# Kernel tuning notes

Measured on AMD Instinct MI355X. Metric: run time of the kernel, lower is better.

Reference implementation:

```python
import jax, jax.numpy as jnp
import numpy as np

K = 17  # pk + 1 (self + 16 neighbors)
NEG_SLOPE = 0.01  # torch LeakyReLU default


def knn_idx(points, k):
    # points: [B, 3, N]; returns nearest-neighbor indices [B, N, k], self first
    inner = -2.0 * jnp.einsum('bcn,bcm->bnm', points, points)
    xx = jnp.sum(points * points, axis=1)  # [B, N]
    pairwise = -xx[:, :, None] - inner - xx[:, None, :]  # -||pi - pj||^2
    _, idx = jax.lax.top_k(pairwise, k)  # largest = nearest; [B, N, k]
    return idx


def gather_edge_features(x, idx):
    # x: [B, C, N], idx: [B, N, k] -> [B, C, k, N]
    g = jax.vmap(lambda xb, ib: xb[:, ib])(x, idx)  # [B, C, N, k]
    return jnp.transpose(g, (0, 1, 3, 2))


def setup_inputs() -> dict:
    key = jax.random.key(0)
    ks = jax.random.split(key, 16)
    B, N = 2, 8192
    Cl, Cg = 64, 1024
    Cef_in = Cl + 3          # 67
    Cmlp_in = Cg + Cl + 128 + 3  # 1219

    def w(k, shape, fan_in):
        return jax.random.normal(k, shape, dtype=jnp.float32) * (1.0 / np.sqrt(fan_in))

    return {
        'global_feat': jax.random.normal(ks[0], (B, Cg), dtype=jnp.float32),
        'points': jax.random.normal(ks[1], (B, 3, N), dtype=jnp.float32),
        'local_feats': jax.random.normal(ks[2], (B, Cl, N), dtype=jnp.float32),
        'W_ef1': w(ks[3], (256, Cef_in), Cef_in),
        'b_ef1': jnp.zeros((256,), jnp.float32),
        'W_ef2': w(ks[4], (128, 256), 256),
        'b_ef2': jnp.zeros((128,), jnp.float32),
        'W1': w(ks[5], (1024, Cmlp_in), Cmlp_in),
        'b1': jnp.zeros((1024,), jnp.float32),
        'W2': w(ks[6], (256, 1024), 1024),
        'b2': jnp.zeros((256,), jnp.float32),
        'W3': w(ks[7], (1, 256), 256),
        'b3': jnp.zeros((1,), jnp.float32),
    }


def reference(global_feat, points, local_feats, W_ef1, b_ef1, W_ef2, b_ef2,
              W1, b1, W2, b2, W3, b3):
    B, _, N = points.shape
    idx = knn_idx(points, K)                       # [B, N, K]
    x_knn = gather_edge_features(points, idx)      # [B, 3, K, N]
    f_knn = gather_edge_features(local_feats, idx) # [B, Cl, K, N]
    # minus_xyz_center=True: center-relative coords for neighbors (skip self slot 0)
    x_knn = jnp.concatenate(
        [x_knn[:, :, :1, :], points[:, :, None, :] - x_knn[:, :, 1:, :]], axis=2)
    # with_xyz=True
    f = jnp.concatenate([f_knn, x_knn], axis=1)    # [B, Cl+3, K, N]
    # ef_mlp: 1x1 Conv2d -> LeakyReLU -> 1x1 Conv2d
    h = jnp.einsum('oc,bckn->bokn', W_ef1, f) + b_ef1[None, :, None, None]
    h = jax.nn.leaky_relu(h, NEG_SLOPE)
    h = jnp.einsum('oc,bckn->bokn', W_ef2, h) + b_ef2[None, :, None, None]
    f_max = jnp.max(h, axis=2)                     # [B, 128, N]
    g = jnp.broadcast_to(global_feat[:, :, None], (B, global_feat.shape[1], N))
    feature = jnp.concatenate([g, local_feats, f_max, points], axis=1)  # [B, 1219, N]
    # mlp: 1x1 Conv1d stack
    y = jnp.einsum('oc,bcn->bon', W1, feature) + b1[None, :, None]
    y = jax.nn.leaky_relu(y, NEG_SLOPE)
    y = jnp.einsum('oc,bcn->bon', W2, y) + b2[None, :, None]
    y = jax.nn.leaky_relu(y, NEG_SLOPE)
    out = jnp.einsum('oc,bcn->bon', W3, y) + b3[None, :, None]  # [B, 1, N]
    return out
```

## Files before the change

### kernel.cpp

```cpp
#include <hip/hip_runtime.h>
#include <hip/hip_bf16.h>
#include <cstdint>

#define B 2
#define N 8192
#define KTOT 17
#define CL 64
#define CEF 67
#define H1 256
#define H2 128
#define CG 1024
#define O1 1024
#define O2 256
#define NCHW 8
#define WCH 256
#define KPAIR 9

typedef unsigned long long u64;
typedef __bf16 bf16x8 __attribute__((ext_vector_type(8)));
typedef float f32x4 __attribute__((ext_vector_type(4)));

__device__ __forceinline__ float lrelu(float v) { return fmaxf(v, 0.01f * v); }

__device__ __forceinline__ unsigned short f2bf(float f) {
    union { float f; unsigned u; } v; v.f = f;
    unsigned r = v.u + 0x7FFFu + ((v.u >> 16) & 1u);
    return (unsigned short)(r >> 16);
}

__device__ __forceinline__ unsigned cvt_pk_bf16(float lo, float hi) {
    unsigned r;
    asm("v_cvt_pk_bf16_f32 %0, %1, %2" : "=v"(r) : "v"(lo), "v"(hi));
    return r;
}

__device__ __forceinline__ float norm3(float x, float y, float z) {
    return __fmaf_rn(z, z, __fmaf_rn(y, y, __fmul_rn(x, x)));
}
__device__ __forceinline__ float dist_key(float qx, float qy, float qz, float qq,
                                          float4 c) {
    float dot = __fmaf_rn(qz, c.z, __fmaf_rn(qy, c.y, __fmul_rn(qx, c.x)));
    float t = __fmaf_rn(-2.f, dot, qq);
    return fmaxf(__fadd_rn(t, c.w), 0.f);
}

__device__ __forceinline__ int nbucket(float nn) {
    return (int)fminf(nn * 16.f, 255.f);
}

__global__ void prep_cand4_hist(const float* __restrict__ pts, float4* __restrict__ cand4,
                                unsigned* __restrict__ hist) {
    int id = blockIdx.x * 256 + threadIdx.x;
    int b = id >> 13, j = id & (N - 1);
    const float* px = pts + (size_t)b * 3 * N;
    float x = px[j], y = px[N + j], z = px[2 * N + j];
    float nn = norm3(x, y, z);
    cand4[id] = make_float4(x, y, z, nn);
    atomicAdd(&hist[b * 256 + nbucket(nn)], 1u);
}

__global__ void knn_prefix(const unsigned* __restrict__ hist, unsigned* __restrict__ boff) {
    __shared__ unsigned s[256];
    int t = threadIdx.x;
    for (int b = 0; b < B; ++b) {
        s[t] = hist[b * 256 + t];
        __syncthreads();
        for (int d = 1; d < 256; d <<= 1) {
            unsigned v = (t >= d) ? s[t - d] : 0u;
            __syncthreads();
            s[t] += v;
            __syncthreads();
        }
        boff[b * 256 + t] = s[t] - hist[b * 256 + t];
        __syncthreads();
    }
}
__global__ void knn_scatter(const float4* __restrict__ cand4, unsigned* __restrict__ boff,
                            float4* __restrict__ cand4s, int* __restrict__ sortidx) {
    int id = blockIdx.x * 256 + threadIdx.x;
    int b = id >> 13, j = id & (N - 1);
    float4 c = cand4[id];
    unsigned pos = atomicAdd(&boff[b * 256 + nbucket(c.w)], 1u);
    cand4s[(size_t)b * N + pos] = c;
    sortidx[b * N + pos] = j;
}

#define S1 24576
#define S2 32768
#define S3 229376
#define S4 262144
__global__ void prepack_all(const float* __restrict__ W_ef1, const float* __restrict__ W_ef2,
                            const float* __restrict__ W1, const float* __restrict__ W2,
                            unsigned short* __restrict__ W1p, unsigned short* __restrict__ W2p,
                            unsigned short* __restrict__ W1m, unsigned short* __restrict__ W2m) {
    int id = blockIdx.x * 256 + threadIdx.x;
    if (id < S1) {
        int j = id & 7, l = (id >> 3) & 63, rest = id >> 9;
        int ks = rest % 3, mt = rest / 3;
        int m = mt * 16 + (l & 15);
        int k = ks * 32 + ((l >> 4) << 3) + j;
        W1p[id] = f2bf((k < CEF) ? W_ef1[m * CEF + k] : 0.f);
        return;
    }
    id -= S1;
    if (id < S2) {
        int j = id & 7, l = (id >> 3) & 63, rest = id >> 9;
        int ks = rest & 7, mt = rest >> 3;
        int m = mt * 16 + (l & 15);
        int k = ks * 32 + ((l >> 4) << 3) + j;
        W2p[id] = f2bf(W_ef2[m * H1 + k]);
        return;
    }
    id -= S2;
    if (id < S3) {
        int j = id & 7, l = (id >> 3) & 63, rest = id >> 9;
        int ks = rest % 7; int rest2 = rest / 7;
        int mt = rest2 & 3, w = (rest2 >> 2) & 3, ch = rest2 >> 4;
        int m = ch * 256 + w * 64 + mt * 16 + (l & 15);
        int k = ks * 32 + ((l >> 4) << 3) + j;
        W1m[id] = (k < 195) ? f2bf(W1[(size_t)m * 1219 + 1024 + k]) : (unsigned short)0;
        return;
    }
    id -= S3;
    if (id < S4) {
        int j = id & 7, l = (id >> 3) & 63, rest = id >> 9;
        int ks = rest & 7; int rest2 = rest >> 3;
        int mt = rest2 & 3, w = (rest2 >> 2) & 3, ch = rest2 >> 4;
        int m = w * 64 + mt * 16 + (l & 15);
        int k = ch * 256 + ks * 32 + ((l >> 4) << 3) + j;
        W2m[id] = f2bf(W2[(size_t)m * 1024 + k]);
    }
}

__global__ void prep_lf_bf(const float* __restrict__ lf, unsigned short* __restrict__ out) {
    int id = blockIdx.x * 256 + threadIdx.x;
    int c = id & 63;
    int n = (id >> 6) & (N - 1);
    int b = id >> 19;
    out[id] = f2bf(lf[((size_t)b * CL + c) * N + n]);
}

__global__ __launch_bounds__(256) void gvec_kernel(const float* __restrict__ W1,
                                                   const float* __restrict__ b1,
                                                   const float* __restrict__ g,
                                                   float* __restrict__ gvec) {
    const int t = threadIdx.x;
    const int l = t & 63;
    const int o = blockIdx.x * 4 + (t >> 6);
    const int b = blockIdx.y;
    const float* row = W1 + (size_t)o * 1219;
    const float* gb = g + b * CG;
    float s = 0.f;
#pragma unroll
    for (int i = 0; i < CG / 64; ++i)
        s = fmaf(row[l + i * 64], gb[l + i * 64], s);
    s += __shfl_xor(s, 1);  s += __shfl_xor(s, 2);  s += __shfl_xor(s, 4);
    s += __shfl_xor(s, 8);  s += __shfl_xor(s, 16); s += __shfl_xor(s, 32);
    if (l == 0) gvec[b * O1 + o] = s + b1[o];
}

__global__ __launch_bounds__(256) void knn_pass1w(const float4* __restrict__ cand4s,
                                                  float* __restrict__ topd) {
    const int t = threadIdx.x;
    const int x = blockIdx.x;
    const int chunk = blockIdx.y;
    const int b = blockIdx.z;
    int wstart = x * 256 - 896;
    wstart = wstart < 0 ? 0 : (wstart > N - 2048 ? N - 2048 : wstart);
    const int p = x * 256 + t;
    const int rel = p - wstart - chunk * WCH;
    const float4 q = cand4s[(size_t)b * N + p];
    const float qq = q.w;
    const float4* cb = cand4s + (size_t)b * N + wstart + chunk * WCH;
    float qd[16];
#pragma unroll
    for (int r = 0; r < 16; ++r) qd[r] = __builtin_inff();
#pragma unroll 8
    for (int s = 0; s < WCH; ++s) {
        float key = dist_key(q.x, q.y, q.z, qq, cb[s]);
        if (s == rel) key = __builtin_inff();
#pragma unroll
        for (int r = 15; r >= 1; --r)
            qd[r] = __builtin_amdgcn_fmed3f(key, qd[r - 1], qd[r]);
        qd[0] = fminf(key, qd[0]);
    }
#pragma unroll
    for (int s = 0; s < 16; ++s)
        topd[(size_t)((b * NCHW + chunk) * 16 + s) * N + p] = qd[s];
}

__global__ __launch_bounds__(256) void knn_thresh(const float* __restrict__ topd,
                                                  float* __restrict__ Tbuf) {
    const int t = threadIdx.x;
    const int i = blockIdx.x * 256 + t;
    const int b = blockIdx.y;
    float qd[16];
#pragma unroll
    for (int s = 0; s < 16; ++s)
        qd[s] = topd[(size_t)((b * NCHW + 0) * 16 + s) * N + i];
    for (int c = 1; c < NCHW; ++c) {
        for (int s = 0; s < 16; ++s) {
            float pk = topd[(size_t)((b * NCHW + c) * 16 + s) * N + i];
            if (pk >= qd[15]) break;
#pragma unroll
            for (int r = 15; r >= 1; --r)
                qd[r] = __builtin_amdgcn_fmed3f(pk, qd[r - 1], qd[r]);
            qd[0] = fminf(pk, qd[0]);
        }
    }
    Tbuf[b * N + i] = qd[15];
}

__global__ __launch_bounds__(256) void knn_recover(const float4* __restrict__ cand4s,
                                                   const int* __restrict__ sortidx,
                                                   const float* __restrict__ Tbuf,
                                                   const unsigned* __restrict__ boff,
                                                   int* __restrict__ idx) {
    const int t = threadIdx.x;
    const int lg = t & 15;
    const int grp = t >> 4;
    const int b = blockIdx.y;
    const int pq = blockIdx.x * 16 + grp;
    __shared__ u64 cbuf[16][64];
    __shared__ unsigned obuf[16][17];
    __shared__ int scnt[16];
    if (lg == 0) scnt[grp] = 0;
    __syncthreads();
    const int gq = sortidx[b * N + pq];
    const float4 q = cand4s[(size_t)b * N + pq];
    const float qq = q.w;
    const float T = Tbuf[b * N + pq];
    const float nq = sqrtf(qq);
    const float r = sqrtf(T) * 1.001f + 0.01f;
    const float lov = (nq > r) ? (nq - r) * (nq - r) : 0.f;
    const float hiv = (nq + r) * (nq + r);
    const int lob = nbucket(lov), hib = nbucket(hiv);
    const int start = (lob == 0) ? 0 : (int)boff[b * 256 + lob - 1];
    const int end = (int)boff[b * 256 + hib];
    const float4* cs = cand4s + (size_t)b * N;
    const int* si = sortidx + b * N;
    const int last = end - 1;
    for (int pos = start + lg; pos < end; pos += 64) {
        int p1 = pos + 16, p2 = pos + 32, p3 = pos + 48;
        float4 c0 = cs[pos];
        float4 c1 = cs[p1 < end ? p1 : last];
        float4 c2 = cs[p2 < end ? p2 : last];
        float4 c3 = cs[p3 < end ? p3 : last];
        float k0 = dist_key(q.x, q.y, q.z, qq, c0);
        float k1 = dist_key(q.x, q.y, q.z, qq, c1);
        float k2 = dist_key(q.x, q.y, q.z, qq, c2);
        float k3 = dist_key(q.x, q.y, q.z, qq, c3);
        if (k0 <= T) {
            int j = si[pos];
            if (j != gq) { int p = atomicAdd(&scnt[grp], 1); if (p < 64) cbuf[grp][p] = ((u64)__float_as_uint(k0) << 32) | (unsigned)j; }
        }
        if (k1 <= T && p1 < end) {
            int j = si[p1];
            if (j != gq) { int p = atomicAdd(&scnt[grp], 1); if (p < 64) cbuf[grp][p] = ((u64)__float_as_uint(k1) << 32) | (unsigned)j; }
        }
        if (k2 <= T && p2 < end) {
            int j = si[p2];
            if (j != gq) { int p = atomicAdd(&scnt[grp], 1); if (p < 64) cbuf[grp][p] = ((u64)__float_as_uint(k2) << 32) | (unsigned)j; }
        }
        if (k3 <= T && p3 < end) {
            int j = si[p3];
            if (j != gq) { int p = atomicAdd(&scnt[grp], 1); if (p < 64) cbuf[grp][p] = ((u64)__float_as_uint(k3) << 32) | (unsigned)j; }
        }
    }
    __syncthreads();
    int cnt = scnt[grp]; if (cnt > 64) cnt = 64;
    u64 mine[4]; bool have[4]; int rank[4];
#pragma unroll
    for (int e = 0; e < 4; ++e) {
        int pi = lg + e * 16;
        have[e] = pi < cnt;
        mine[e] = have[e] ? cbuf[grp][pi] : ~0ull;
        rank[e] = 0;
    }
    for (int m = 0; m < cnt; ++m) {
        u64 v = cbuf[grp][m];
#pragma unroll
        for (int e = 0; e < 4; ++e) rank[e] += (v < mine[e]) ? 1 : 0;
    }
    obuf[grp][1 + lg] = (unsigned)gq;
    __syncthreads();
#pragma unroll
    for (int e = 0; e < 4; ++e)
        if (have[e] && rank[e] < 16)
            obuf[grp][1 + rank[e]] = (unsigned)(mine[e] & 0xFFFFFFFFu);
    if (lg == 0) obuf[grp][0] = (unsigned)gq;
    __syncthreads();
    int* op = idx + (size_t)(b * N + gq) * KTOT;
    op[lg] = (int)obuf[grp][lg];
    if (lg == 0) op[16] = (int)obuf[grp][16];
}

__global__ __launch_bounds__(256) void ef_mlp_mfma(
        const unsigned short* __restrict__ lfb16, const float4* __restrict__ cand4,
        const int* __restrict__ idx,
        const unsigned short* __restrict__ W1p, const float* __restrict__ b_ef1,
        const unsigned short* __restrict__ W2p, const float* __restrict__ b_ef2,
        unsigned short* __restrict__ fmax_bf) {
    const int t = threadIdx.x;
    const int w = t >> 6;
    const int l = t & 63;
    const int n0 = blockIdx.x * 16;
    const int b = blockIdx.y;

    __shared__ unsigned short f_lds[32][104];
    __shared__ unsigned short h1_lds[32][264];
    __shared__ int idx_l[16][17];

    for (int e = t; e < 16 * 17; e += 256) {
        int p = e / 17, k = e - p * 17;
        idx_l[p][k] = idx[(size_t)(b * N + n0 + p) * KTOT + k];
    }
    for (int e = t; e < 32 * 29; e += 256) {
        int col = e / 29, rr = 67 + e % 29;
        f_lds[col][rr] = 0;
    }

    f32x4 b1i[4];
#pragma unroll
    for (int mt = 0; mt < 4; ++mt)
#pragma unroll
        for (int r = 0; r < 4; ++r)
            b1i[mt][r] = b_ef1[(w * 4 + mt) * 16 + ((l >> 4) << 2) + r];
    f32x4 b2i[2];
#pragma unroll
    for (int i = 0; i < 2; ++i)
#pragma unroll
        for (int r = 0; r < 4; ++r)
            b2i[i][r] = b_ef2[(w * 2 + i) * 16 + ((l >> 4) << 2) + r];

    bf16x8 A1[12];
#pragma unroll
    for (int mt = 0; mt < 4; ++mt)
#pragma unroll
        for (int ks = 0; ks < 3; ++ks)
            A1[mt * 3 + ks] = *(const bf16x8*)(W1p + (size_t)(((w * 4 + mt) * 3 + ks) * 64 + l) * 8);
    bf16x8 A2[16];
#pragma unroll
    for (int i = 0; i < 2; ++i)
#pragma unroll
        for (int ks = 0; ks < 8; ++ks)
            A2[i * 8 + ks] = *(const bf16x8*)(W2p + (size_t)(((w * 2 + i) * 8 + ks) * 64 + l) * 8);

    const int p_my = t >> 4;
    const int cbr = (t & 15) * 4;
    const unsigned short* lfb = lfb16 + (size_t)b * N * 64;
    const float4* cand4b = cand4 + (size_t)b * N;
    float selfp = 0.f;
    if (t < 48) selfp = ((const float*)(cand4b + n0 + (t & 15)))[t >> 4];

    __syncthreads();

    uint2 rbf[2];
    float rp[2];
    auto prefetch = [&](int g) {
#pragma unroll
        for (int sl = 0; sl < 2; ++sl) {
            int kk = 2 * g + sl; if (kk > 16) kk = 16;
            int j = idx_l[p_my][kk];
            rbf[sl] = *(const uint2*)(lfb + (size_t)j * 64 + cbr);
        }
        if (t < 48) {
#pragma unroll
            for (int sl = 0; sl < 2; ++sl) {
                int kk = 2 * g + sl; if (kk > 16) kk = 16;
                int j = idx_l[t & 15][kk];
                rp[sl] = ((const float*)(cand4b + j))[t >> 4];
            }
        }
    };
    auto commit = [&](int g) {
#pragma unroll
        for (int sl = 0; sl < 2; ++sl)
            *(uint2*)&f_lds[sl * 16 + p_my][cbr] = rbf[sl];
        if (t < 48) {
#pragma unroll
            for (int sl = 0; sl < 2; ++sl) {
                int kk = 2 * g + sl; if (kk > 16) kk = 16;
                float v = (kk == 0) ? selfp : selfp - rp[sl];
                f_lds[sl * 16 + (t & 15)][64 + (t >> 4)] = f2bf(v);
            }
        }
    };

    prefetch(0);
    f32x4 rmax[2];
#pragma unroll
    for (int i = 0; i < 2; ++i)
#pragma unroll
        for (int r = 0; r < 4; ++r) rmax[i][r] = -1e30f;

    for (int g = 0; g < KPAIR; ++g) {
        commit(g);
        __syncthreads();
        if (g < KPAIR - 1) prefetch(g + 1);
        f32x4 acc1[4][2];
#pragma unroll
        for (int mt = 0; mt < 4; ++mt)
#pragma unroll
            for (int nt = 0; nt < 2; ++nt) acc1[mt][nt] = b1i[mt];
#pragma unroll
        for (int nt = 0; nt < 2; ++nt) {
            const int col = nt * 16 + (l & 15);
            bf16x8 Bf0 = *(const bf16x8*)&f_lds[col][(l >> 4) * 8];
            bf16x8 Bf1 = *(const bf16x8*)&f_lds[col][32 + (l >> 4) * 8];
            bf16x8 Bf2 = *(const bf16x8*)&f_lds[col][64 + (l >> 4) * 8];
#pragma unroll
            for (int mt = 0; mt < 4; ++mt) {
                acc1[mt][nt] = __builtin_amdgcn_mfma_f32_16x16x32_bf16(A1[mt * 3 + 0], Bf0, acc1[mt][nt], 0, 0, 0);
                acc1[mt][nt] = __builtin_amdgcn_mfma_f32_16x16x32_bf16(A1[mt * 3 + 1], Bf1, acc1[mt][nt], 0, 0, 0);
                acc1[mt][nt] = __builtin_amdgcn_mfma_f32_16x16x32_bf16(A1[mt * 3 + 2], Bf2, acc1[mt][nt], 0, 0, 0);
            }
        }
#pragma unroll
        for (int mt = 0; mt < 4; ++mt)
#pragma unroll
            for (int nt = 0; nt < 2; ++nt) {
                uint2 d;
                d.x = cvt_pk_bf16(lrelu(acc1[mt][nt][0]), lrelu(acc1[mt][nt][1]));
                d.y = cvt_pk_bf16(lrelu(acc1[mt][nt][2]), lrelu(acc1[mt][nt][3]));
                *(uint2*)&h1_lds[nt * 16 + (l & 15)][(w * 4 + mt) * 16 + ((l >> 4) << 2)] = d;
            }
        __syncthreads();
        f32x4 acc2[2][2];
#pragma unroll
        for (int i = 0; i < 2; ++i)
#pragma unroll
            for (int nt = 0; nt < 2; ++nt) acc2[i][nt] = b2i[i];
#pragma unroll
        for (int nt = 0; nt < 2; ++nt) {
            const int col = nt * 16 + (l & 15);
#pragma unroll
            for (int ks = 0; ks < 8; ++ks) {
                bf16x8 Bf = *(const bf16x8*)&h1_lds[col][ks * 32 + (l >> 4) * 8];
                acc2[0][nt] = __builtin_amdgcn_mfma_f32_16x16x32_bf16(A2[0 * 8 + ks], Bf, acc2[0][nt], 0, 0, 0);
                acc2[1][nt] = __builtin_amdgcn_mfma_f32_16x16x32_bf16(A2[1 * 8 + ks], Bf, acc2[1][nt], 0, 0, 0);
            }
        }
#pragma unroll
        for (int i = 0; i < 2; ++i)
#pragma unroll
            for (int nt = 0; nt < 2; ++nt)
#pragma unroll
                for (int r = 0; r < 4; ++r)
                    rmax[i][r] = fmaxf(rmax[i][r], acc2[i][nt][r]);
    }
    const size_t nbase = ((size_t)(b * N + n0 + (l & 15))) * H2;
#pragma unroll
    for (int i = 0; i < 2; ++i) {
        uint2 d;
        d.x = cvt_pk_bf16(rmax[i][0], rmax[i][1]);
        d.y = cvt_pk_bf16(rmax[i][2], rmax[i][3]);
        *(uint2*)&fmax_bf[nbase + (w * 2 + i) * 16 + ((l >> 4) << 2)] = d;
    }
}

__global__ __launch_bounds__(512) void mlp_mfma(
        const unsigned short* __restrict__ lfb16, const float* __restrict__ pts,
        const unsigned short* __restrict__ fmax_bf, const float* __restrict__ gvec,
        const unsigned short* __restrict__ W1m, const unsigned short* __restrict__ W2m,
        const float* __restrict__ W3, const float* __restrict__ b2v,
        const float* __restrict__ b3v, float* __restrict__ out) {
    const int t = threadIdx.x;
    const int w2 = t >> 6;
    const int l = t & 63;
    const int ow = w2 >> 1;
    const int n0 = blockIdx.x * 32;
    const int b = blockIdx.y;

    __shared__ unsigned short feat_s[32 * 256];
    __shared__ unsigned short y1c_s[32 * 256];
    __shared__ float red[8][32];

    auto sw = [](int n, int cbyte) -> unsigned {
        return (unsigned)(n << 9) | ((unsigned)cbyte ^ (((unsigned)n & 7u) << 4));
    };
    char* featB = (char*)feat_s;
    char* y1cB = (char*)y1c_s;

    const unsigned short* lfb = lfb16 + (size_t)b * N * 64;
    for (int e = t; e < 32 * 64; e += 512) {
        int c = e & 63, n = e >> 6;
        *(unsigned short*)(featB + sw(n, c * 2)) = lfb[(size_t)(n0 + n) * 64 + c];
    }
    for (int e = t; e < 32 * 128; e += 512) {
        int c = e & 127, n = e >> 7;
        *(unsigned short*)(featB + sw(n, (64 + c) * 2)) =
            fmax_bf[((size_t)(b * N + n0 + n)) * H2 + c];
    }
    if (t < 96) {
        int n = t & 31, d = t >> 5;
        *(unsigned short*)(featB + sw(n, (192 + d) * 2)) =
            f2bf(pts[((size_t)(b * 3 + d)) * N + n0 + n]);
    }
    for (int e = t; e < 32 * 29; e += 512) {
        int n = e / 29, c = 195 + e % 29;
        *(unsigned short*)(featB + sw(n, c * 2)) = 0;
    }
    __syncthreads();

    f32x4 accB[2][2];
#pragma unroll
    for (int mt = 0; mt < 2; ++mt)
#pragma unroll
        for (int nt = 0; nt < 2; ++nt)
            accB[mt][nt] = (f32x4){0.f, 0.f, 0.f, 0.f};

    for (int ch = 0; ch < 4; ++ch) {
        bf16x8 A1[2][7];
#pragma unroll
        for (int mt = 0; mt < 2; ++mt) {
            const int omt = (w2 & 1) * 2 + mt;
#pragma unroll
            for (int ks = 0; ks < 7; ++ks)
                A1[mt][ks] = *(const bf16x8*)(W1m +
                    (size_t)((((ch * 4 + ow) * 4 + omt) * 7 + ks) * 64 + l) * 8);
        }
        f32x4 accA[2][2];
#pragma unroll
        for (int mt = 0; mt < 2; ++mt) {
            const int m = w2 * 32 + mt * 16 + ((l >> 4) << 2);
            const f32x4 gv = *(const f32x4*)(gvec + b * O1 + ch * 256 + m);
#pragma unroll
            for (int nt = 0; nt < 2; ++nt)
                accA[mt][nt] = gv;
        }
#pragma unroll
        for (int nt = 0; nt < 2; ++nt) {
            const int n = nt * 16 + (l & 15);
#pragma unroll
            for (int ks = 0; ks < 7; ++ks) {
                bf16x8 Bf = *(const bf16x8*)(featB + sw(n, ks * 64 + (l >> 4) * 16));
#pragma unroll
                for (int mt = 0; mt < 2; ++mt)
                    accA[mt][nt] = __builtin_amdgcn_mfma_f32_16x16x32_bf16(
                        A1[mt][ks], Bf, accA[mt][nt], 0, 0, 0);
            }
        }
        bf16x8 A2[2][8];
#pragma unroll
        for (int mt = 0; mt < 2; ++mt) {
            const int omt = (w2 & 1) * 2 + mt;
#pragma unroll
            for (int ks = 0; ks < 8; ++ks)
                A2[mt][ks] = *(const bf16x8*)(W2m +
                    (size_t)((((ch * 4 + ow) * 4 + omt) * 8 + ks) * 64 + l) * 8);
        }
        if (ch) __syncthreads();
#pragma unroll
        for (int mt = 0; mt < 2; ++mt) {
            const int m = w2 * 32 + mt * 16 + ((l >> 4) << 2);
#pragma unroll
            for (int nt = 0; nt < 2; ++nt) {
                const int n = nt * 16 + (l & 15);
                uint2 d;
                d.x = cvt_pk_bf16(lrelu(accA[mt][nt][0]), lrelu(accA[mt][nt][1]));
                d.y = cvt_pk_bf16(lrelu(accA[mt][nt][2]), lrelu(accA[mt][nt][3]));
                *(uint2*)(y1cB + sw(n, m * 2)) = d;
            }
        }
        __syncthreads();
#pragma unroll
        for (int nt = 0; nt < 2; ++nt) {
            const int n = nt * 16 + (l & 15);
#pragma unroll
            for (int ks = 0; ks < 8; ++ks) {
                bf16x8 Bf = *(const bf16x8*)(y1cB + sw(n, ks * 64 + (l >> 4) * 16));
#pragma unroll
                for (int mt = 0; mt < 2; ++mt)
                    accB[mt][nt] = __builtin_amdgcn_mfma_f32_16x16x32_bf16(
                        A2[mt][ks], Bf, accB[mt][nt], 0, 0, 0);
            }
        }
    }

    float p0 = 0.f, p1 = 0.f;
#pragma unroll
    for (int mt = 0; mt < 2; ++mt) {
        const int m = w2 * 32 + mt * 16 + ((l >> 4) << 2);
        const f32x4 bb = *(const f32x4*)(b2v + m);
        const f32x4 w3 = *(const f32x4*)(W3 + m);
#pragma unroll
        for (int r = 0; r < 4; ++r) {
            p0 = fmaf(w3[r], lrelu(accB[mt][0][r] + bb[r]), p0);
            p1 = fmaf(w3[r], lrelu(accB[mt][1][r] + bb[r]), p1);
        }
    }
    p0 += __shfl_xor(p0, 16); p0 += __shfl_xor(p0, 32);
    p1 += __shfl_xor(p1, 16); p1 += __shfl_xor(p1, 32);
    if (l < 16) { red[w2][l] = p0; red[w2][16 + l] = p1; }
    __syncthreads();
    if (t < 32) {
        float s = b3v[0];
#pragma unroll
        for (int ww = 0; ww < 8; ++ww) s += red[ww][t];
        out[(size_t)b * N + n0 + t] = s;
    }
}

extern "C" void kernel_launch(void* const* d_in, const int* in_sizes, int n_in,
                              void* d_out, int out_size, void* d_ws, size_t ws_size,
                              hipStream_t stream) {
    const float* g     = (const float*)d_in[0];
    const float* pts   = (const float*)d_in[1];
    const float* lf    = (const float*)d_in[2];
    const float* W_ef1 = (const float*)d_in[3];
    const float* b_ef1 = (const float*)d_in[4];
    const float* W_ef2 = (const float*)d_in[5];
    const float* b_ef2 = (const float*)d_in[6];
    const float* W1    = (const float*)d_in[7];
    const float* b1    = (const float*)d_in[8];
    const float* W2    = (const float*)d_in[9];
    const float* b2    = (const float*)d_in[10];
    const float* W3    = (const float*)d_in[11];
    const float* b3    = (const float*)d_in[12];
    float* out = (float*)d_out;

    char* ws = (char*)d_ws;
    int*      idx     = (int*)ws;     ws += (size_t)B * N * KTOT * 4;
    float4*   cand4   = (float4*)ws;  ws += (size_t)B * N * 16;
    float4*   cand4s  = (float4*)ws;  ws += (size_t)B * N * 16;
    int*      sortidx = (int*)ws;     ws += (size_t)B * N * 4;
    unsigned* hist    = (unsigned*)ws; ws += (size_t)B * 256 * 4;
    unsigned* boff    = (unsigned*)ws; ws += (size_t)B * 256 * 4;
    float*    topd    = (float*)ws;
    unsigned short* fmax_bf = (unsigned short*)topd;
    ws += (size_t)B * NCHW * 16 * N * 4;
    float*    Tbuf  = (float*)ws;    ws += (size_t)B * N * 4;
    float*    gvec  = (float*)ws;    ws += (size_t)B * O1 * 4;
    unsigned short* lfb16 = (unsigned short*)ws; ws += (size_t)B * N * 64 * 2;
    unsigned short* W1p = (unsigned short*)ws; ws += (size_t)S1 * 2;
    unsigned short* W2p = (unsigned short*)ws; ws += (size_t)S2 * 2;
    unsigned short* W1m = (unsigned short*)ws; ws += (size_t)S3 * 2;
    unsigned short* W2m = (unsigned short*)ws; ws += (size_t)S4 * 2;

    hipMemsetAsync(hist, 0, (size_t)B * 256 * 4, stream);
    prep_cand4_hist<<<dim3((B * N) / 256), 256, 0, stream>>>(pts, cand4, hist);
    prep_lf_bf<<<dim3((B * N * 64) / 256), 256, 0, stream>>>(lf, lfb16);
    prepack_all<<<dim3((S1 + S2 + S3 + S4) / 256), 256, 0, stream>>>(
        W_ef1, W_ef2, W1, W2, W1p, W2p, W1m, W2m);
    gvec_kernel<<<dim3(O1 / 4, B), 256, 0, stream>>>(W1, b1, g, gvec);
    knn_prefix<<<dim3(1), 256, 0, stream>>>(hist, boff);
    knn_scatter<<<dim3((B * N) / 256), 256, 0, stream>>>(cand4, boff, cand4s, sortidx);
    knn_pass1w<<<dim3(N / 256, NCHW, B), 256, 0, stream>>>(cand4s, topd);
    knn_thresh<<<dim3(N / 256, B), 256, 0, stream>>>(topd, Tbuf);
    knn_recover<<<dim3(N / 16, B), 256, 0, stream>>>(cand4s, sortidx, Tbuf, boff, idx);
    ef_mlp_mfma<<<dim3(N / 16, B), 256, 0, stream>>>(lfb16, cand4, idx, W1p, b_ef1, W2p, b_ef2, fmax_bf);
    mlp_mfma<<<dim3(N / 32, B), 512, 0, stream>>>(lfb16, pts, fmax_bf, gvec, W1m, W2m, W3, b2, b3, out);
}
```

Measured before the change: 200.8 us.

## Load gathered edge features straight into MFMA registers and double-buffer h1

The edge-feature MLP kernel no longer stages gathered neighbor features through a shared-memory tile. Each lane now loads its own bf16x8 B-fragments directly from global memory and builds the xyz-offset fragment in registers. The h1 tile is double-buffered, which removes one block-wide barrier per neighbor pair. The cost is that the software prefetch is dropped, so the global gather latency now sits right before the MFMAs and each wave re-gathers the same neighbor rows redundantly.

```diff
diff --git a/kernel.cpp b/kernel.cpp
--- a/kernel.cpp
+++ b/kernel.cpp
@@ -304,34 +304,31 @@
     const int t = threadIdx.x;
     const int w = t >> 6;
     const int l = t & 63;
+    const int hi = l >> 4;
+    const int col = l & 15;
     const int n0 = blockIdx.x * 16;
     const int b = blockIdx.y;
 
-    __shared__ unsigned short f_lds[32][104];
-    __shared__ unsigned short h1_lds[32][264];
+    __shared__ unsigned short h1_lds[2][32][264];
     __shared__ int idx_l[16][17];
 
     for (int e = t; e < 16 * 17; e += 256) {
         int p = e / 17, k = e - p * 17;
         idx_l[p][k] = idx[(size_t)(b * N + n0 + p) * KTOT + k];
     }
-    for (int e = t; e < 32 * 29; e += 256) {
-        int col = e / 29, rr = 67 + e % 29;
-        f_lds[col][rr] = 0;
-    }
 
     f32x4 b1i[4];
 #pragma unroll
     for (int mt = 0; mt < 4; ++mt)
 #pragma unroll
         for (int r = 0; r < 4; ++r)
-            b1i[mt][r] = b_ef1[(w * 4 + mt) * 16 + ((l >> 4) << 2) + r];
+            b1i[mt][r] = b_ef1[(w * 4 + mt) * 16 + (hi << 2) + r];
     f32x4 b2i[2];
 #pragma unroll
     for (int i = 0; i < 2; ++i)
 #pragma unroll
         for (int r = 0; r < 4; ++r)
-            b2i[i][r] = b_ef2[(w * 2 + i) * 16 + ((l >> 4) << 2) + r];
+            b2i[i][r] = b_ef2[(w * 2 + i) * 16 + (hi << 2) + r];
 
     bf16x8 A1[12];
 #pragma unroll
@@ -346,76 +343,58 @@
         for (int ks = 0; ks < 8; ++ks)
             A2[i * 8 + ks] = *(const bf16x8*)(W2p + (size_t)(((w * 2 + i) * 8 + ks) * 64 + l) * 8);
 
-    const int p_my = t >> 4;
-    const int cbr = (t & 15) * 4;
     const unsigned short* lfb = lfb16 + (size_t)b * N * 64;
     const float4* cand4b = cand4 + (size_t)b * N;
-    float selfp = 0.f;
-    if (t < 48) selfp = ((const float*)(cand4b + n0 + (t & 15)))[t >> 4];
+    const float4 selfc = cand4b[n0 + col];
 
     __syncthreads();
 
-    uint2 rbf[2];
-    float rp[2];
-    auto prefetch = [&](int g) {
-#pragma unroll
-        for (int sl = 0; sl < 2; ++sl) {
-            int kk = 2 * g + sl; if (kk > 16) kk = 16;
-            int j = idx_l[p_my][kk];
-            rbf[sl] = *(const uint2*)(lfb + (size_t)j * 64 + cbr);
-        }
-        if (t < 48) {
-#pragma unroll
-            for (int sl = 0; sl < 2; ++sl) {
-                int kk = 2 * g + sl; if (kk > 16) kk = 16;
-                int j = idx_l[t & 15][kk];
-                rp[sl] = ((const float*)(cand4b + j))[t >> 4];
+    f32x4 rmax[2];
+#pragma unroll
+    for (int i = 0; i < 2; ++i)
+#pragma unroll
+        for (int r = 0; r < 4; ++r) rmax[i][r] = -1e30f;
+
+    int buf = 0;
+    for (int g = 0; g < KPAIR; ++g) {
+        bf16x8 B0[2], B1[2], B2[2];
+        int jj[2];
+#pragma unroll
+        for (int nt = 0; nt < 2; ++nt) {
+            int kk = 2 * g + nt; if (kk > 16) kk = 16;
+            jj[nt] = idx_l[col][kk];
+            const unsigned short* base = lfb + (size_t)jj[nt] * 64 + hi * 8;
+            B0[nt] = *(const bf16x8*)base;
+            B1[nt] = *(const bf16x8*)(base + 32);
+        }
+#pragma unroll
+        for (int nt = 0; nt < 2; ++nt) {
+            int kk = 2 * g + nt; if (kk > 16) kk = 16;
+            union { unsigned u[4]; bf16x8 v; } z;
+            z.u[0] = 0; z.u[1] = 0; z.u[2] = 0; z.u[3] = 0;
+            if (hi == 0) {
+                float4 nb = cand4b[jj[nt]];
+                float dx = (kk == 0) ? selfc.x : selfc.x - nb.x;
+                float dy = (kk == 0) ? selfc.y : selfc.y - nb.y;
+                float dz = (kk == 0) ? selfc.z : selfc.z - nb.z;
+                z.u[0] = cvt_pk_bf16(dx, dy);
+                z.u[1] = cvt_pk_bf16(dz, 0.f);
             }
-        }
-    };
-    auto commit = [&](int g) {
-#pragma unroll
-        for (int sl = 0; sl < 2; ++sl)
-            *(uint2*)&f_lds[sl * 16 + p_my][cbr] = rbf[sl];
-        if (t < 48) {
-#pragma unroll
-            for (int sl = 0; sl < 2; ++sl) {
-                int kk = 2 * g + sl; if (kk > 16) kk = 16;
-                float v = (kk == 0) ? selfp : selfp - rp[sl];
-                f_lds[sl * 16 + (t & 15)][64 + (t >> 4)] = f2bf(v);
+            B2[nt] = z.v;
+        }
+        f32x4 acc1[4][2];
+#pragma unroll
+        for (int mt = 0; mt < 4; ++mt)
+#pragma unroll
+            for (int nt = 0; nt < 2; ++nt) acc1[mt][nt] = b1i[mt];
+#pragma unroll
+        for (int nt = 0; nt < 2; ++nt)
+#pragma unroll
+            for (int mt = 0; mt < 4; ++mt) {
+                acc1[mt][nt] = __builtin_amdgcn_mfma_f32_16x16x32_bf16(A1[mt * 3 + 0], B0[nt], acc1[mt][nt], 0, 0, 0);
+                acc1[mt][nt] = __builtin_amdgcn_mfma_f32_16x16x32_bf16(A1[mt * 3 + 1], B1[nt], acc1[mt][nt], 0, 0, 0);
+                acc1[mt][nt] = __builtin_amdgcn_mfma_f32_16x16x32_bf16(A1[mt * 3 + 2], B2[nt], acc1[mt][nt], 0, 0, 0);
             }
-        }
-    };
-
-    prefetch(0);
-    f32x4 rmax[2];
-#pragma unroll
-    for (int i = 0; i < 2; ++i)
-#pragma unroll
-        for (int r = 0; r < 4; ++r) rmax[i][r] = -1e30f;
-
-    for (int g = 0; g < KPAIR; ++g) {
-        commit(g);
-        __syncthreads();
-        if (g < KPAIR - 1) prefetch(g + 1);
-        f32x4 acc1[4][2];
-#pragma unroll
-        for (int mt = 0; mt < 4; ++mt)
-#pragma unroll
-            for (int nt = 0; nt < 2; ++nt) acc1[mt][nt] = b1i[mt];
-#pragma unroll
-        for (int nt = 0; nt < 2; ++nt) {
-            const int col = nt * 16 + (l & 15);
-            bf16x8 Bf0 = *(const bf16x8*)&f_lds[col][(l >> 4) * 8];
-            bf16x8 Bf1 = *(const bf16x8*)&f_lds[col][32 + (l >> 4) * 8];
-            bf16x8 Bf2 = *(const bf16x8*)&f_lds[col][64 + (l >> 4) * 8];
-#pragma unroll
-            for (int mt = 0; mt < 4; ++mt) {
-                acc1[mt][nt] = __builtin_amdgcn_mfma_f32_16x16x32_bf16(A1[mt * 3 + 0], Bf0, acc1[mt][nt], 0, 0, 0);
-                acc1[mt][nt] = __builtin_amdgcn_mfma_f32_16x16x32_bf16(A1[mt * 3 + 1], Bf1, acc1[mt][nt], 0, 0, 0);
-                acc1[mt][nt] = __builtin_amdgcn_mfma_f32_16x16x32_bf16(A1[mt * 3 + 2], Bf2, acc1[mt][nt], 0, 0, 0);
-            }
-        }
 #pragma unroll
         for (int mt = 0; mt < 4; ++mt)
 #pragma unroll
@@ -423,7 +402,7 @@
                 uint2 d;
                 d.x = cvt_pk_bf16(lrelu(acc1[mt][nt][0]), lrelu(acc1[mt][nt][1]));
                 d.y = cvt_pk_bf16(lrelu(acc1[mt][nt][2]), lrelu(acc1[mt][nt][3]));
-                *(uint2*)&h1_lds[nt * 16 + (l & 15)][(w * 4 + mt) * 16 + ((l >> 4) << 2)] = d;
+                *(uint2*)&h1_lds[buf][nt * 16 + col][(w * 4 + mt) * 16 + (hi << 2)] = d;
             }
         __syncthreads();
         f32x4 acc2[2][2];
@@ -433,10 +412,10 @@
             for (int nt = 0; nt < 2; ++nt) acc2[i][nt] = b2i[i];
 #pragma unroll
         for (int nt = 0; nt < 2; ++nt) {
-            const int col = nt * 16 + (l & 15);
+            const int colr = nt * 16 + col;
 #pragma unroll
             for (int ks = 0; ks < 8; ++ks) {
-                bf16x8 Bf = *(const bf16x8*)&h1_lds[col][ks * 32 + (l >> 4) * 8];
+                bf16x8 Bf = *(const bf16x8*)&h1_lds[buf][colr][ks * 32 + hi * 8];
                 acc2[0][nt] = __builtin_amdgcn_mfma_f32_16x16x32_bf16(A2[0 * 8 + ks], Bf, acc2[0][nt], 0, 0, 0);
                 acc2[1][nt] = __builtin_amdgcn_mfma_f32_16x16x32_bf16(A2[1 * 8 + ks], Bf, acc2[1][nt], 0, 0, 0);
             }
@@ -448,14 +427,15 @@
 #pragma unroll
                 for (int r = 0; r < 4; ++r)
                     rmax[i][r] = fmaxf(rmax[i][r], acc2[i][nt][r]);
-    }
-    const size_t nbase = ((size_t)(b * N + n0 + (l & 15))) * H2;
+        buf ^= 1;
+    }
+    const size_t nbase = ((size_t)(b * N + n0 + col)) * H2;
 #pragma unroll
     for (int i = 0; i < 2; ++i) {
         uint2 d;
         d.x = cvt_pk_bf16(rmax[i][0], rmax[i][1]);
         d.y = cvt_pk_bf16(rmax[i][2], rmax[i][3]);
-        *(uint2*)&fmax_bf[nbase + (w * 2 + i) * 16 + ((l >> 4) << 2)] = d;
+        *(uint2*)&fmax_bf[nbase + (w * 2 + i) * 16 + (hi << 2)] = d;
     }
 }
 
```

Result: slower. 213.7 us (+6.4%).
